# Performance work log

Hardware: AMD Instinct MI355X
Metric: run time of the kernel (lower is better)

Reference implementation:

```python
import jax, jax.numpy as jnp
import numpy as np

B, S, D, H, V, C = 4, 2048, 1024, 16, 32000, 10
FFN_DIM = 2 * D
HD = D // H
SCALE = float(np.sqrt(HD))


def _posenc(seq, d):
    pos = jnp.arange(seq, dtype=jnp.float32)[:, None]
    div = jnp.exp(jnp.arange(0, d, 2, dtype=jnp.float32) * (-np.log(10000.0) / d))
    pe = jnp.zeros((seq, d), dtype=jnp.float32)
    pe = pe.at[:, 0::2].set(jnp.sin(pos * div))
    pe = pe.at[:, 1::2].set(jnp.cos(pos * div))
    return pe


def _layernorm(x, g, b, eps=1e-5):
    mu = jnp.mean(x, axis=-1, keepdims=True)
    var = jnp.mean(jnp.square(x - mu), axis=-1, keepdims=True)
    return (x - mu) * jax.lax.rsqrt(var + eps) * g + b


def setup_inputs() -> dict:
    key = jax.random.key(0)
    ks = jax.random.split(key, 10)
    x_ids = jax.random.randint(ks[0], (B, S), 0, V, dtype=jnp.int64 if jax.config.jax_enable_x64 else jnp.int32)
    mask = jnp.ones((B, S), dtype=jnp.int32)
    emb = (jax.random.normal(ks[1], (V, D), jnp.float32) * 0.02).at[0].set(0.0)  # padding_idx=0
    qkv_w = jax.random.normal(ks[2], (3 * D, D), jnp.float32) * 0.02
    fc_w = jax.random.normal(ks[3], (D, D), jnp.float32) * 0.02
    fc_b = jnp.zeros((D,), jnp.float32)
    ln1_g = jnp.ones((D,), jnp.float32); ln1_b = jnp.zeros((D,), jnp.float32)
    ffn_w1 = jax.random.normal(ks[4], (FFN_DIM, D), jnp.float32) * 0.02
    ffn_b1 = jnp.zeros((FFN_DIM,), jnp.float32)
    ffn_w2 = jax.random.normal(ks[5], (D, FFN_DIM), jnp.float32) * 0.02
    ffn_b2 = jnp.zeros((D,), jnp.float32)
    ln2_g = jnp.ones((D,), jnp.float32); ln2_b = jnp.zeros((D,), jnp.float32)
    pr_w1 = jax.random.normal(ks[6], (D, D), jnp.float32) * 0.02
    pr_b1 = jnp.zeros((D,), jnp.float32)
    pr_w2 = jax.random.normal(ks[7], (C, D), jnp.float32) * 0.02
    pr_b2 = jnp.zeros((C,), jnp.float32)
    return dict(x_ids=x_ids, mask=mask, emb=emb, qkv_w=qkv_w, fc_w=fc_w, fc_b=fc_b,
                ln1_g=ln1_g, ln1_b=ln1_b, ffn_w1=ffn_w1, ffn_b1=ffn_b1,
                ffn_w2=ffn_w2, ffn_b2=ffn_b2, ln2_g=ln2_g, ln2_b=ln2_b,
                pr_w1=pr_w1, pr_b1=pr_b1, pr_w2=pr_w2, pr_b2=pr_b2)


def reference(x_ids, mask, emb, qkv_w, fc_w, fc_b, ln1_g, ln1_b,
              ffn_w1, ffn_b1, ffn_w2, ffn_b2, ln2_g, ln2_b,
              pr_w1, pr_b1, pr_w2, pr_b2):
    # embedding + absolute positional encoding
    x = emb[x_ids] + _posenc(S, D)  # [B,S,D]
    residual = x
    # multi-head attention (dropout is identity at eval)
    qkv = jnp.einsum('bsd,ed->bse', x, qkv_w)  # [B,S,3D]
    q, k, v = jnp.split(qkv, 3, axis=-1)
    q = q.reshape(B, S, H, HD)
    k = k.reshape(B, S, H, HD)
    v = v.reshape(B, S, H, HD)
    attn = jnp.einsum('bqhd,bkhd->bhqk', q, k) / SCALE  # [B,H,S,S]
    attn = jnp.where(mask[:, None, None, :] == 0, -jnp.inf, attn)
    attn = jax.nn.softmax(attn, axis=-1)
    o = jnp.einsum('bhqk,bkhd->bqhd', attn, v).reshape(B, S, D)
    o = jnp.einsum('bsd,ed->bse', o, fc_w) + fc_b
    x = _layernorm(o + residual, ln1_g, ln1_b)
    # FFN block (residual + LayerNorm inside)
    h = jax.nn.gelu(jnp.einsum('bsd,fd->bsf', x, ffn_w1) + ffn_b1, approximate=False)
    h = jnp.einsum('bsf,df->bsd', h, ffn_w2) + ffn_b2
    x = _layernorm(h + x, ln2_g, ln2_b)
    # masked max-pool over sequence
    x = jnp.where(mask[:, :, None] == 0, -jnp.inf, x).max(axis=1)  # [B,D]
    # prediction head
    h = jax.nn.gelu(x @ pr_w1.T + pr_b1, approximate=False)
    logits = h @ pr_w2.T + pr_b2  # [B,C]
    return logits
```

## Files before the change

kernel.cpp:

```cpp
#include <hip/hip_runtime.h>
#include <math.h>

#define B_   4
#define S_   2048
#define D_   1024
#define H_   16
#define HD_  64
#define C_   10
#define FFN_ 2048
#define M_   (B_ * S_)
#define D3_  (3 * D_)

typedef unsigned short u16;
typedef __bf16 bf16x8 __attribute__((ext_vector_type(8)));
typedef float  f32x4  __attribute__((ext_vector_type(4)));

__device__ __forceinline__ u16 f2bf(float f) {
  union { float f; unsigned u; } x; x.f = f;
  unsigned r = x.u + 0x7fffu + ((x.u >> 16) & 1u);
  return (u16)(r >> 16);
}
__device__ __forceinline__ float bf2f(u16 h) {
  union { unsigned u; float f; } x; x.u = ((unsigned)h) << 16;
  return x.f;
}
__device__ __forceinline__ unsigned pkbf(float a, float b) {
  union { float f; unsigned u; } x, y; x.f = a; y.f = b;
  return __builtin_amdgcn_perm(y.u + 0x8000u, x.u + 0x8000u, 0x07060302u);
}
__device__ __forceinline__ float gelu_f(float x) {
  return 0.5f * x * (1.f + erff(x * 0.70710678118654752440f));
}
__device__ __forceinline__ void gload_lds16(const void* g, void* l) {
  __builtin_amdgcn_global_load_lds(
      (const __attribute__((address_space(1))) unsigned int*)g,
      (__attribute__((address_space(3))) unsigned int*)l, 16, 0, 0);
}

__global__ __launch_bounds__(256) void cvt_kernel(const float* __restrict__ src,
                                                  u16* __restrict__ dst, int n) {
  const int i = (blockIdx.x * 256 + threadIdx.x) * 4;
  if (i >= n) return;
  f32x4 v = *(const f32x4*)&src[i];
  ushort4 o;
  o.x = f2bf(v[0]); o.y = f2bf(v[1]); o.z = f2bf(v[2]); o.w = f2bf(v[3]);
  *(ushort4*)&dst[i] = o;
}

__global__ __launch_bounds__(256) void embed_kernel(const int* __restrict__ ids,
                                                    const float* __restrict__ emb,
                                                    float* __restrict__ resid,
                                                    u16* __restrict__ xb) {
  const int m  = blockIdx.x;
  const int s  = m & (S_ - 1);
  const int id = ids[m];
  const int d0 = threadIdx.x * 4;
#pragma unroll
  for (int k = 0; k < 4; ++k) {
    const int d   = d0 + k;
    const float e = emb[(size_t)id * D_ + d];
    const float fr  = expf((float)(d & ~1) * (-9.210340371976184f / 1024.0f));
    const float ang = (float)s * fr;
    const float pe  = (d & 1) ? cosf(ang) : sinf(ang);
    const float v   = e + pe;
    resid[(size_t)m * D_ + d] = v;
    xb[(size_t)m * D_ + d]    = f2bf(v);
  }
}

template <int BIAS, int GELU, int OUTBF, int VSPLIT>
__global__ __launch_bounds__(256) void gemm_bt(const u16* __restrict__ A,
                                               const u16* __restrict__ W,
                                               const float* __restrict__ bias,
                                               float* __restrict__ outf,
                                               u16* __restrict__ outb,
                                               u16* __restrict__ vt,
                                               int M, int N, int K) {
  __shared__ u16 As[128 * 32];
  __shared__ u16 Bs[128 * 32];
  const int tid  = threadIdx.x;
  const int lane = tid & 63;
  const int w    = tid >> 6;
  const int bx   = blockIdx.x, by = blockIdx.y;
  const int lr   = lane >> 2;
  const int lc   = (lane & 3) * 8;
  const u16* Ag0 = A + (size_t)(by * 128 + w * 16 + lr) * K + lc;
  const u16* Wg0 = W + (size_t)(bx * 128 + w * 16 + lr) * K + lc;
  u16* As0 = &As[(w * 16) * 32];
  u16* As1 = &As[(64 + w * 16) * 32];
  u16* Bs0 = &Bs[(w * 16) * 32];
  u16* Bs1 = &Bs[(64 + w * 16) * 32];
  const size_t K64 = (size_t)64 * K;

  f32x4 acc[4][4] = {};
  const int wr  = (w & 1) * 64;
  const int wc  = (w >> 1) * 64;
  const int fr  = lane & 15;
  const int fko = (lane >> 4) * 8;

  for (int kt = 0; kt < K; kt += 32) {
    gload_lds16(Ag0 + kt, As0);
    gload_lds16(Ag0 + K64 + kt, As1);
    gload_lds16(Wg0 + kt, Bs0);
    gload_lds16(Wg0 + K64 + kt, Bs1);
    __syncthreads();
    bf16x8 af[4], bfr[4];
#pragma unroll
    for (int i = 0; i < 4; ++i)
      af[i] = *(const bf16x8*)&As[(wr + i * 16 + fr) * 32 + fko];
#pragma unroll
    for (int j = 0; j < 4; ++j)
      bfr[j] = *(const bf16x8*)&Bs[(wc + j * 16 + fr) * 32 + fko];
#pragma unroll
    for (int i = 0; i < 4; ++i)
#pragma unroll
      for (int j = 0; j < 4; ++j)
        acc[i][j] = __builtin_amdgcn_mfma_f32_16x16x32_bf16(af[i], bfr[j], acc[i][j], 0, 0, 0);
    __syncthreads();
  }

  const int er = (lane >> 4) * 4;
  const int ec = lane & 15;
  if (VSPLIT && bx >= 16) {
#pragma unroll
    for (int i = 0; i < 4; ++i) {
      const int gm0 = by * 128 + wr + i * 16 + er;
      const int bb  = gm0 >> 11;
      const int s0  = gm0 & (S_ - 1);
#pragma unroll
      for (int j = 0; j < 4; ++j) {
        const int dcol = bx * 128 + wc + j * 16 + ec - 2 * D_;
        const int hh = dcol >> 6, dd = dcol & 63;
        ushort4 pk;
        pk.x = f2bf(acc[i][j][0]); pk.y = f2bf(acc[i][j][1]);
        pk.z = f2bf(acc[i][j][2]); pk.w = f2bf(acc[i][j][3]);
        *(ushort4*)&vt[((size_t)((bb * H_ + hh) * 64 + dd)) * S_ + s0] = pk;
      }
    }
    return;
  }
#pragma unroll
  for (int i = 0; i < 4; ++i) {
#pragma unroll
    for (int j = 0; j < 4; ++j) {
      const int gn = bx * 128 + wc + j * 16 + ec;
      const float bv = BIAS ? bias[gn] : 0.f;
#pragma unroll
      for (int r = 0; r < 4; ++r) {
        const int gm = by * 128 + wr + i * 16 + er + r;
        float v = acc[i][j][r] + bv;
        if (GELU) v = gelu_f(v);
        if (OUTBF) outb[(size_t)gm * N + gn] = f2bf(v);
        else       outf[(size_t)gm * N + gn] = v;
      }
    }
  }
}

__device__ __forceinline__ bf16x8 ldsfrag(const u16* buf, int rowbase, int fr, int kb) {
  return *(const bf16x8*)&buf[(rowbase + fr) * 64 + ((kb ^ (fr & 7)) << 3)];
}

__global__ __launch_bounds__(256) void attn_mfma_kernel(const u16* __restrict__ qkv,
                                                        const u16* __restrict__ vt,
                                                        const int* __restrict__ mask,
                                                        u16* __restrict__ attno) {
  __shared__ u16 Qs[128 * 64];
  __shared__ u16 Ks[64 * 64];
  __shared__ u16 Vts[64 * 64];
  __shared__ u16 Ps[4][32 * 64];
  __shared__ float mb[64];
  const int tid = threadIdx.x, lane = tid & 63, w = tid >> 6;
  const int b = blockIdx.z, h = blockIdx.y, qt = blockIdx.x;
  const int l3 = lane >> 3;
  const int sb = (lane & 7) ^ (l3 & 7);
  const int fr = lane & 15, fq = lane >> 4;

  {
    const u16* qbase = qkv + (size_t)(b * S_ + qt * 128 + w * 32) * D3_ + h * 64 + sb * 8;
#pragma unroll
    for (int c = 0; c < 4; ++c)
      gload_lds16(qbase + (size_t)(c * 8 + l3) * D3_, &Qs[(w * 32 + c * 8) * 64]);
  }

  float m_st[2] = {-3e38f, -3e38f};
  float l_st[2] = {0.f, 0.f};
  f32x4 ot[4][2] = {};
  u16* PsW = Ps[w];

  for (int kt = 0; kt < S_ / 64; ++kt) {
    __syncthreads();
    {
      const u16* kbase = qkv + (size_t)(b * S_ + kt * 64 + w * 16) * D3_ + D_ + h * 64 + sb * 8;
      gload_lds16(kbase + (size_t)l3 * D3_, &Ks[(w * 16) * 64]);
      gload_lds16(kbase + (size_t)(8 + l3) * D3_, &Ks[(w * 16 + 8) * 64]);
      const u16* vbase = vt + ((size_t)((b * H_ + h) * 64 + w * 16)) * S_ + kt * 64 + sb * 8;
      gload_lds16(vbase + (size_t)l3 * S_, &Vts[(w * 16) * 64]);
      gload_lds16(vbase + (size_t)(8 + l3) * S_, &Vts[(w * 16 + 8) * 64]);
    }
    if (tid < 64) mb[tid] = (mask[b * S_ + kt * 64 + tid] != 0) ? 0.f : -1e30f;
    __syncthreads();

    f32x4 sf[4][2] = {};
#pragma unroll
    for (int ks = 0; ks < 2; ++ks) {
      const int kb = ks * 4 + fq;
      bf16x8 qf0 = ldsfrag(Qs, w * 32, fr, kb);
      bf16x8 qf1 = ldsfrag(Qs, w * 32 + 16, fr, kb);
#pragma unroll
      for (int r4 = 0; r4 < 4; ++r4) {
        bf16x8 kf = ldsfrag(Ks, r4 * 16, fr, kb);
        sf[r4][0] = __builtin_amdgcn_mfma_f32_16x16x32_bf16(kf, qf0, sf[r4][0], 0, 0, 0);
        sf[r4][1] = __builtin_amdgcn_mfma_f32_16x16x32_bf16(kf, qf1, sf[r4][1], 0, 0, 0);
      }
    }
#pragma unroll
    for (int r4 = 0; r4 < 4; ++r4) {
      const f32x4 vb = *(const f32x4*)&mb[r4 * 16 + fq * 4];
      sf[r4][0] += vb;
      sf[r4][1] += vb;
    }

#pragma unroll
    for (int i = 0; i < 2; ++i) {
      float mt = fmaxf(fmaxf(fmaxf(sf[0][i][0], sf[0][i][1]), fmaxf(sf[0][i][2], sf[0][i][3])),
                 fmaxf(fmaxf(fmaxf(sf[1][i][0], sf[1][i][1]), fmaxf(sf[1][i][2], sf[1][i][3])),
                 fmaxf(fmaxf(fmaxf(sf[2][i][0], sf[2][i][1]), fmaxf(sf[2][i][2], sf[2][i][3])),
                       fmaxf(fmaxf(sf[3][i][0], sf[3][i][1]), fmaxf(sf[3][i][2], sf[3][i][3])))));
      mt = fmaxf(mt, __shfl_xor(mt, 16));
      mt = fmaxf(mt, __shfl_xor(mt, 32));
      const float mo = m_st[i];
      const float mn = fmaxf(mo, mt);
      const float alpha = __expf((mo - mn) * 0.125f);
      const int prow = i * 16 + fr;
      u16* pw = PsW + prow * 64;
      float sum = 0.f;
#pragma unroll
      for (int r4 = 0; r4 < 4; ++r4) {
        const float p0 = __expf((sf[r4][i][0] - mn) * 0.125f);
        const float p1 = __expf((sf[r4][i][1] - mn) * 0.125f);
        const float p2 = __expf((sf[r4][i][2] - mn) * 0.125f);
        const float p3 = __expf((sf[r4][i][3] - mn) * 0.125f);
        sum += (p0 + p1) + (p2 + p3);
        const int bk0 = 2 * r4 + (fq >> 1);
        const int off = ((bk0 ^ (prow & 7)) << 3) + ((fq & 1) << 2);
        uint2 pk; pk.x = pkbf(p0, p1); pk.y = pkbf(p2, p3);
        *(uint2*)&pw[off] = pk;
      }
      sum += __shfl_xor(sum, 16);
      sum += __shfl_xor(sum, 32);
      l_st[i] = l_st[i] * alpha + sum;
      m_st[i] = mn;
#pragma unroll
      for (int db = 0; db < 4; ++db) ot[db][i] *= alpha;
    }
    asm volatile("s_waitcnt lgkmcnt(0)" ::: "memory");

#pragma unroll
    for (int ks = 0; ks < 2; ++ks) {
      const int kb = ks * 4 + fq;
      bf16x8 pf0 = ldsfrag(PsW, 0, fr, kb);
      bf16x8 pf1 = ldsfrag(PsW, 16, fr, kb);
#pragma unroll
      for (int db = 0; db < 4; ++db) {
        bf16x8 vf = ldsfrag(Vts, db * 16, fr, kb);
        ot[db][0] = __builtin_amdgcn_mfma_f32_16x16x32_bf16(vf, pf0, ot[db][0], 0, 0, 0);
        ot[db][1] = __builtin_amdgcn_mfma_f32_16x16x32_bf16(vf, pf1, ot[db][1], 0, 0, 0);
      }
    }
  }

#pragma unroll
  for (int i = 0; i < 2; ++i) {
    const float l = l_st[i];
    const float inv = (l > 0.f) ? 1.f / l : 0.f;
    const int qrow = qt * 128 + w * 32 + i * 16 + fr;
    u16* dst = attno + (size_t)(b * S_ + qrow) * D_ + h * 64 + fq * 4;
#pragma unroll
    for (int db = 0; db < 4; ++db) {
      ushort4 pk;
      pk.x = f2bf(ot[db][i][0] * inv);
      pk.y = f2bf(ot[db][i][1] * inv);
      pk.z = f2bf(ot[db][i][2] * inv);
      pk.w = f2bf(ot[db][i][3] * inv);
      *(ushort4*)&dst[db * 16] = pk;
    }
  }
}

__global__ __launch_bounds__(256) void ln_kernel(const float* __restrict__ a,
                                                 const float* __restrict__ res,
                                                 const float* __restrict__ g,
                                                 const float* __restrict__ be,
                                                 float* __restrict__ outf,
                                                 u16* __restrict__ outb) {
  const int row = blockIdx.x, tid = threadIdx.x;
  const int lane = tid & 63, w = tid >> 6;
  const size_t base = (size_t)row * D_ + tid * 4;
  const f32x4 va = *(const f32x4*)(a + base);
  const f32x4 vr = *(const f32x4*)(res + base);
  const f32x4 v  = va + vr;
  float s = v[0] + v[1] + v[2] + v[3];
#pragma unroll
  for (int o = 32; o > 0; o >>= 1) s += __shfl_xor(s, o);
  __shared__ float red[8];
  if (lane == 0) red[w] = s;
  __syncthreads();
  const float mu = (red[0] + red[1] + red[2] + red[3]) * (1.f / D_);
  const f32x4 d = v - mu;
  float s2 = d[0] * d[0] + d[1] * d[1] + d[2] * d[2] + d[3] * d[3];
#pragma unroll
  for (int o = 32; o > 0; o >>= 1) s2 += __shfl_xor(s2, o);
  if (lane == 0) red[4 + w] = s2;
  __syncthreads();
  const float var = (red[4] + red[5] + red[6] + red[7]) * (1.f / D_);
  const float rs = rsqrtf(var + 1e-5f);
#pragma unroll
  for (int k = 0; k < 4; ++k) {
    const int ch = tid * 4 + k;
    const float y = d[k] * rs * g[ch] + be[ch];
    outf[base + k] = y;
    outb[base + k] = f2bf(y);
  }
}

__global__ __launch_bounds__(256) void pool_part_kernel(const float* __restrict__ x,
                                                        const int* __restrict__ mask,
                                                        float* __restrict__ part) {
  const int b = blockIdx.y, ch = blockIdx.x;
  const int d0 = threadIdx.x * 4;
  f32x4 acc = {-INFINITY, -INFINITY, -INFINITY, -INFINITY};
  for (int ss = 0; ss < 64; ++ss) {
    const int s = ch * 64 + ss;
    if (mask[b * S_ + s] != 0) {
      const f32x4 v = *(const f32x4*)&x[(size_t)(b * S_ + s) * D_ + d0];
      acc[0] = fmaxf(acc[0], v[0]);
      acc[1] = fmaxf(acc[1], v[1]);
      acc[2] = fmaxf(acc[2], v[2]);
      acc[3] = fmaxf(acc[3], v[3]);
    }
  }
  *(f32x4*)&part[(size_t)(b * 32 + ch) * D_ + d0] = acc;
}
__global__ __launch_bounds__(256) void pool_final_kernel(const float* __restrict__ part,
                                                         float* __restrict__ pooled) {
  const int b = blockIdx.x;
  const int d0 = threadIdx.x * 4;
  f32x4 acc = {-INFINITY, -INFINITY, -INFINITY, -INFINITY};
  for (int ch = 0; ch < 32; ++ch) {
    const f32x4 v = *(const f32x4*)&part[(size_t)(b * 32 + ch) * D_ + d0];
    acc[0] = fmaxf(acc[0], v[0]);
    acc[1] = fmaxf(acc[1], v[1]);
    acc[2] = fmaxf(acc[2], v[2]);
    acc[3] = fmaxf(acc[3], v[3]);
  }
  *(f32x4*)&pooled[(size_t)b * D_ + d0] = acc;
}

__global__ __launch_bounds__(256) void head1_kernel(const float* __restrict__ pooled,
                                                    const float* __restrict__ w,
                                                    const float* __restrict__ bias,
                                                    float* __restrict__ hh) {
  const int lane = threadIdx.x & 63;
  const int gw = blockIdx.x * 4 + (threadIdx.x >> 6);
  const int b = gw >> 10, n = gw & 1023;
  const float* p  = pooled + b * 1024;
  const float* wr = w + (size_t)n * 1024;
  float s = 0.f;
  for (int d = lane; d < 1024; d += 64) s += p[d] * wr[d];
#pragma unroll
  for (int off = 32; off > 0; off >>= 1) s += __shfl_xor(s, off);
  if (lane == 0) hh[b * 1024 + n] = gelu_f(s + bias[n]);
}
__global__ __launch_bounds__(256) void head2_kernel(const float* __restrict__ hh,
                                                    const float* __restrict__ w,
                                                    const float* __restrict__ bias,
                                                    float* __restrict__ out) {
  const int lane = threadIdx.x & 63;
  const int gw = blockIdx.x * 4 + (threadIdx.x >> 6);
  const int b = gw / 10, c = gw % 10;
  const float* p  = hh + b * 1024;
  const float* wr = w + (size_t)c * 1024;
  float s = 0.f;
  for (int d = lane; d < 1024; d += 64) s += p[d] * wr[d];
#pragma unroll
  for (int off = 32; off > 0; off >>= 1) s += __shfl_xor(s, off);
  if (lane == 0) out[b * 10 + c] = s + bias[c];
}

#define OFF_RESID  0UL
#define OFF_F1     33554432UL
#define OFF_XB     67108864UL
#define OFF_QKVB   83886080UL
#define OFF_ATTNO  134217728UL
#define OFF_WQKV   150994944UL
#define OFF_WFC    157286400UL
#define OFF_WF1    159383552UL
#define OFF_WF2    163577856UL
#define OFF_PART   167772160UL
#define OFF_POOLED 168296448UL
#define OFF_HH     168312832UL

extern "C" void kernel_launch(void* const* d_in, const int* in_sizes, int n_in,
                              void* d_out, int out_size, void* d_ws, size_t ws_size,
                              hipStream_t stream) {
  const int*   x_ids  = (const int*)d_in[0];
  const int*   mask   = (const int*)d_in[1];
  const float* emb    = (const float*)d_in[2];
  const float* qkv_w  = (const float*)d_in[3];
  const float* fc_w   = (const float*)d_in[4];
  const float* fc_b   = (const float*)d_in[5];
  const float* ln1_g  = (const float*)d_in[6];
  const float* ln1_b  = (const float*)d_in[7];
  const float* ffn_w1 = (const float*)d_in[8];
  const float* ffn_b1 = (const float*)d_in[9];
  const float* ffn_w2 = (const float*)d_in[10];
  const float* ffn_b2 = (const float*)d_in[11];
  const float* ln2_g  = (const float*)d_in[12];
  const float* ln2_b  = (const float*)d_in[13];
  const float* pr_w1  = (const float*)d_in[14];
  const float* pr_b1  = (const float*)d_in[15];
  const float* pr_w2  = (const float*)d_in[16];
  const float* pr_b2  = (const float*)d_in[17];
  float* out = (float*)d_out;
  char* ws = (char*)d_ws;

  float* resid  = (float*)(ws + OFF_RESID);
  float* f1     = (float*)(ws + OFF_F1);
  u16*   vtb    = (u16*)(ws + OFF_F1);
  u16*   xb     = (u16*)(ws + OFF_XB);
  u16*   qkvb   = (u16*)(ws + OFF_QKVB);
  u16*   hb     = (u16*)(ws + OFF_QKVB);
  u16*   attnob = (u16*)(ws + OFF_ATTNO);
  u16*   wqkvb  = (u16*)(ws + OFF_WQKV);
  u16*   wfcb   = (u16*)(ws + OFF_WFC);
  u16*   wf1b   = (u16*)(ws + OFF_WF1);
  u16*   wf2b   = (u16*)(ws + OFF_WF2);
  float* part   = (float*)(ws + OFF_PART);
  float* pooled = (float*)(ws + OFF_POOLED);
  float* hh     = (float*)(ws + OFF_HH);

  cvt_kernel<<<3072, 256, 0, stream>>>(qkv_w,  wqkvb, 3 * D_ * D_);
  cvt_kernel<<<1024, 256, 0, stream>>>(fc_w,   wfcb,  D_ * D_);
  cvt_kernel<<<2048, 256, 0, stream>>>(ffn_w1, wf1b,  FFN_ * D_);
  cvt_kernel<<<2048, 256, 0, stream>>>(ffn_w2, wf2b,  D_ * FFN_);

  embed_kernel<<<M_, 256, 0, stream>>>(x_ids, emb, resid, xb);

  gemm_bt<0, 0, 1, 1><<<dim3(D3_ / 128, M_ / 128), 256, 0, stream>>>(
      xb, wqkvb, nullptr, nullptr, qkvb, vtb, M_, D3_, D_);

  attn_mfma_kernel<<<dim3(S_ / 128, H_, B_), 256, 0, stream>>>(qkvb, vtb, mask, attnob);

  gemm_bt<1, 0, 0, 0><<<dim3(D_ / 128, M_ / 128), 256, 0, stream>>>(
      attnob, wfcb, fc_b, f1, nullptr, nullptr, M_, D_, D_);

  ln_kernel<<<M_, 256, 0, stream>>>(f1, resid, ln1_g, ln1_b, resid, xb);

  gemm_bt<1, 1, 1, 0><<<dim3(FFN_ / 128, M_ / 128), 256, 0, stream>>>(
      xb, wf1b, ffn_b1, nullptr, hb, nullptr, M_, FFN_, D_);

  gemm_bt<1, 0, 0, 0><<<dim3(D_ / 128, M_ / 128), 256, 0, stream>>>(
      hb, wf2b, ffn_b2, f1, nullptr, nullptr, M_, D_, FFN_);

  ln_kernel<<<M_, 256, 0, stream>>>(f1, resid, ln2_g, ln2_b, f1, xb);

  pool_part_kernel<<<dim3(32, B_), 256, 0, stream>>>(f1, mask, part);
  pool_final_kernel<<<B_, 256, 0, stream>>>(part, pooled);

  head1_kernel<<<1024, 256, 0, stream>>>(pooled, pr_w1, pr_b1, hh);
  head2_kernel<<<10, 256, 0, stream>>>(hh, pr_w2, pr_b2, out);
}
```

Before: 699.1 us.

## Widen GEMM K-tile to 64 with swizzled LDS, remap attention grid, use exp2

The GEMM now stages 64-wide K tiles into an XOR-swizzled LDS layout and runs two MFMA sub-steps per barrier. This halves the number of sync points and is meant to reduce LDS bank conflicts, at the cost of more shared memory per block. The attention launch becomes a 1D grid with a custom block-to-(b,h,qt) mapping meant to change scheduling locality across XCDs. The softmax now calls exp2 with a prescaled log2e constant in place of __expf.

```diff
diff --git a/kernel.cpp b/kernel.cpp
--- a/kernel.cpp
+++ b/kernel.cpp
@@ -20,10 +20,6 @@
   unsigned r = x.u + 0x7fffu + ((x.u >> 16) & 1u);
   return (u16)(r >> 16);
 }
-__device__ __forceinline__ float bf2f(u16 h) {
-  union { unsigned u; float f; } x; x.u = ((unsigned)h) << 16;
-  return x.f;
-}
 __device__ __forceinline__ unsigned pkbf(float a, float b) {
   union { float f; unsigned u; } x, y; x.f = a; y.f = b;
   return __builtin_amdgcn_perm(y.u + 0x8000u, x.u + 0x8000u, 0x07060302u);
@@ -35,6 +31,9 @@
   __builtin_amdgcn_global_load_lds(
       (const __attribute__((address_space(1))) unsigned int*)g,
       (__attribute__((address_space(3))) unsigned int*)l, 16, 0, 0);
+}
+__device__ __forceinline__ bf16x8 ldsfrag(const u16* buf, int rowbase, int fr, int kb) {
+  return *(const bf16x8*)&buf[(rowbase + fr) * 64 + ((kb ^ (fr & 7)) << 3)];
 }
 
 __global__ __launch_bounds__(256) void cvt_kernel(const float* __restrict__ src,
@@ -76,51 +75,49 @@
                                                u16* __restrict__ outb,
                                                u16* __restrict__ vt,
                                                int M, int N, int K) {
-  __shared__ u16 As[128 * 32];
-  __shared__ u16 Bs[128 * 32];
+  __shared__ u16 As[128 * 64];
+  __shared__ u16 Bs[128 * 64];
   const int tid  = threadIdx.x;
   const int lane = tid & 63;
   const int w    = tid >> 6;
   const int bx   = blockIdx.x, by = blockIdx.y;
-  const int lr   = lane >> 2;
-  const int lc   = (lane & 3) * 8;
-  const u16* Ag0 = A + (size_t)(by * 128 + w * 16 + lr) * K + lc;
-  const u16* Wg0 = W + (size_t)(bx * 128 + w * 16 + lr) * K + lc;
-  u16* As0 = &As[(w * 16) * 32];
-  u16* As1 = &As[(64 + w * 16) * 32];
-  u16* Bs0 = &Bs[(w * 16) * 32];
-  u16* Bs1 = &Bs[(64 + w * 16) * 32];
-  const size_t K64 = (size_t)64 * K;
+  const int l3   = lane >> 3;
+  const int sb   = (lane & 7) ^ l3;
+  const u16* Ag0 = A + (size_t)(by * 128 + w * 32 + l3) * K + sb * 8;
+  const u16* Wg0 = W + (size_t)(bx * 128 + w * 32 + l3) * K + sb * 8;
 
   f32x4 acc[4][4] = {};
   const int wr  = (w & 1) * 64;
   const int wc  = (w >> 1) * 64;
   const int fr  = lane & 15;
-  const int fko = (lane >> 4) * 8;
-
-  for (int kt = 0; kt < K; kt += 32) {
-    gload_lds16(Ag0 + kt, As0);
-    gload_lds16(Ag0 + K64 + kt, As1);
-    gload_lds16(Wg0 + kt, Bs0);
-    gload_lds16(Wg0 + K64 + kt, Bs1);
+  const int fq  = lane >> 4;
+
+  for (int kt = 0; kt < K; kt += 64) {
+#pragma unroll
+    for (int c = 0; c < 4; ++c) {
+      gload_lds16(Ag0 + (size_t)(c * 8) * K + kt, &As[(w * 32 + c * 8) * 64]);
+      gload_lds16(Wg0 + (size_t)(c * 8) * K + kt, &Bs[(w * 32 + c * 8) * 64]);
+    }
     __syncthreads();
-    bf16x8 af[4], bfr[4];
-#pragma unroll
-    for (int i = 0; i < 4; ++i)
-      af[i] = *(const bf16x8*)&As[(wr + i * 16 + fr) * 32 + fko];
-#pragma unroll
-    for (int j = 0; j < 4; ++j)
-      bfr[j] = *(const bf16x8*)&Bs[(wc + j * 16 + fr) * 32 + fko];
-#pragma unroll
-    for (int i = 0; i < 4; ++i)
-#pragma unroll
-      for (int j = 0; j < 4; ++j)
-        acc[i][j] = __builtin_amdgcn_mfma_f32_16x16x32_bf16(af[i], bfr[j], acc[i][j], 0, 0, 0);
+#pragma unroll
+    for (int ks = 0; ks < 2; ++ks) {
+      const int kb = ks * 4 + fq;
+      bf16x8 af[4], bfr[4];
+#pragma unroll
+      for (int i = 0; i < 4; ++i) af[i] = ldsfrag(As, wr + i * 16, fr, kb);
+#pragma unroll
+      for (int j = 0; j < 4; ++j) bfr[j] = ldsfrag(Bs, wc + j * 16, fr, kb);
+#pragma unroll
+      for (int i = 0; i < 4; ++i)
+#pragma unroll
+        for (int j = 0; j < 4; ++j)
+          acc[i][j] = __builtin_amdgcn_mfma_f32_16x16x32_bf16(af[i], bfr[j], acc[i][j], 0, 0, 0);
+    }
     __syncthreads();
   }
 
-  const int er = (lane >> 4) * 4;
-  const int ec = lane & 15;
+  const int er = fq * 4;
+  const int ec = fr;
   if (VSPLIT && bx >= 16) {
 #pragma unroll
     for (int i = 0; i < 4; ++i) {
@@ -157,9 +154,7 @@
   }
 }
 
-__device__ __forceinline__ bf16x8 ldsfrag(const u16* buf, int rowbase, int fr, int kb) {
-  return *(const bf16x8*)&buf[(rowbase + fr) * 64 + ((kb ^ (fr & 7)) << 3)];
-}
+#define EXPSCL 0.18033688011112042f
 
 __global__ __launch_bounds__(256) void attn_mfma_kernel(const u16* __restrict__ qkv,
                                                         const u16* __restrict__ vt,
@@ -171,9 +166,12 @@
   __shared__ u16 Ps[4][32 * 64];
   __shared__ float mb[64];
   const int tid = threadIdx.x, lane = tid & 63, w = tid >> 6;
-  const int b = blockIdx.z, h = blockIdx.y, qt = blockIdx.x;
+  const int id = blockIdx.x;
+  const int qt = (id >> 3) & 15;
+  const int bh = (id & 7) * 8 + (id >> 7);
+  const int b = bh >> 4, h = bh & 15;
   const int l3 = lane >> 3;
-  const int sb = (lane & 7) ^ (l3 & 7);
+  const int sb = (lane & 7) ^ l3;
   const int fr = lane & 15, fq = lane >> 4;
 
   {
@@ -231,16 +229,16 @@
       mt = fmaxf(mt, __shfl_xor(mt, 32));
       const float mo = m_st[i];
       const float mn = fmaxf(mo, mt);
-      const float alpha = __expf((mo - mn) * 0.125f);
+      const float alpha = __builtin_exp2f((mo - mn) * EXPSCL);
       const int prow = i * 16 + fr;
       u16* pw = PsW + prow * 64;
       float sum = 0.f;
 #pragma unroll
       for (int r4 = 0; r4 < 4; ++r4) {
-        const float p0 = __expf((sf[r4][i][0] - mn) * 0.125f);
-        const float p1 = __expf((sf[r4][i][1] - mn) * 0.125f);
-        const float p2 = __expf((sf[r4][i][2] - mn) * 0.125f);
-        const float p3 = __expf((sf[r4][i][3] - mn) * 0.125f);
+        const float p0 = __builtin_exp2f((sf[r4][i][0] - mn) * EXPSCL);
+        const float p1 = __builtin_exp2f((sf[r4][i][1] - mn) * EXPSCL);
+        const float p2 = __builtin_exp2f((sf[r4][i][2] - mn) * EXPSCL);
+        const float p3 = __builtin_exp2f((sf[r4][i][3] - mn) * EXPSCL);
         sum += (p0 + p1) + (p2 + p3);
         const int bk0 = 2 * r4 + (fq >> 1);
         const int off = ((bk0 ^ (prow & 7)) << 3) + ((fq & 1) << 2);
@@ -450,7 +448,7 @@
   gemm_bt<0, 0, 1, 1><<<dim3(D3_ / 128, M_ / 128), 256, 0, stream>>>(
       xb, wqkvb, nullptr, nullptr, qkvb, vtb, M_, D3_, D_);
 
-  attn_mfma_kernel<<<dim3(S_ / 128, H_, B_), 256, 0, stream>>>(qkvb, vtb, mask, attnob);
+  attn_mfma_kernel<<<1024, 256, 0, stream>>>(qkvb, vtb, mask, attnob);
 
   gemm_bt<1, 0, 0, 0><<<dim3(D_ / 128, M_ / 128), 256, 0, stream>>>(
       attnob, wfcb, fc_b, f1, nullptr, nullptr, M_, D_, D_);
```

Measured after the change: 669.1 us. -4.3%, faster.
